# Kernel tuning notes

Hardware: AMD Instinct MI355X
Metric: run time of the kernel (lower is better)

## Reference

```python
import jax, jax.numpy as jnp
import numpy as np

B, T, H, NC = 64, 512, 1000, 2000
WV, PV, IV, TV, MV = 100000, 50, 5, 20, 500
FEAT = 300 + 4 * 50  # 500
EPS = 1e-5


def setup_inputs() -> dict:
    key = jax.random.key(0)
    ks = jax.random.split(key, 32)

    def emb(k, v, d):
        t = jax.random.normal(k, (v, d), jnp.float32) * 0.1
        return t.at[0].set(0.0)  # padding_idx=0

    def unif(k, shape, s):
        return jax.random.uniform(k, shape, jnp.float32, -s, s)

    s = 1.0 / np.sqrt(H)
    inp = {}
    inp['word_idxs'] = jax.random.randint(ks[0], (B, T), 0, WV)
    inp['pos_idxs'] = jax.random.randint(ks[1], (B, T), 0, PV)
    inp['iob_idxs'] = jax.random.randint(ks[2], (B, T), 0, IV)
    inp['type_idxs'] = jax.random.randint(ks[3], (B, T), 0, TV)
    inp['mention_idxs'] = jax.random.randint(ks[4], (B, T), 0, MV)
    lengths = jnp.sort(jax.random.randint(ks[5], (B,), 1, T + 1))[::-1]
    inp['lengths'] = lengths.at[0].set(T)  # descending, max == T
    inp['hidden'] = jnp.zeros((2, B, H), jnp.float32)
    inp['word_emb'] = emb(ks[6], WV, 300)
    inp['pos_emb'] = emb(ks[7], PV, 50)
    inp['iob_emb'] = emb(ks[8], IV, 50)
    inp['type_emb'] = emb(ks[9], TV, 50)
    inp['mention_emb'] = emb(ks[10], MV, 50)
    inp['w_ih_fwd'] = unif(ks[11], (3 * H, FEAT), s)
    inp['w_hh_fwd'] = unif(ks[12], (3 * H, H), s)
    inp['b_ih_fwd'] = unif(ks[13], (3 * H,), s)
    inp['b_hh_fwd'] = unif(ks[14], (3 * H,), s)
    inp['w_ih_bwd'] = unif(ks[15], (3 * H, FEAT), s)
    inp['w_hh_bwd'] = unif(ks[16], (3 * H, H), s)
    inp['b_ih_bwd'] = unif(ks[17], (3 * H,), s)
    inp['b_hh_bwd'] = unif(ks[18], (3 * H,), s)
    inp['lin_w'] = unif(ks[19], (NC, 2 * H), 1.0 / np.sqrt(2 * H))
    inp['lin_b'] = unif(ks[20], (NC,), 1.0 / np.sqrt(2 * H))
    inp['bn_gamma'] = 1.0 + 0.1 * jax.random.normal(ks[21], (NC,), jnp.float32)
    inp['bn_beta'] = 0.1 * jax.random.normal(ks[22], (NC,), jnp.float32)
    inp['bn_mean'] = 0.1 * jax.random.normal(ks[23], (NC,), jnp.float32)
    inp['bn_var'] = jax.random.uniform(ks[24], (NC,), jnp.float32, 0.5, 1.5)
    return inp


def _gru_dir(x_proj, mask, h0, w_hh, b_hh):
    """x_proj: [T,B,3H] precomputed input projections; mask: [T,B] validity."""
    def step(h, tm):
        xp, m = tm
        hp = h @ w_hh.T + b_hh  # [B,3H]
        xr, xz, xn = jnp.split(xp, 3, axis=-1)
        hr, hz, hn = jnp.split(hp, 3, axis=-1)
        r = jax.nn.sigmoid(xr + hr)
        z = jax.nn.sigmoid(xz + hz)
        n = jnp.tanh(xn + r * hn)
        h_new = (1.0 - z) * n + z * h
        h = jnp.where(m[:, None], h_new, h)  # freeze past sequence end (packed semantics)
        return h, None
    hT, _ = jax.lax.scan(step, h0, (x_proj, mask))
    return hT


def reference(word_idxs, pos_idxs, iob_idxs, type_idxs, mention_idxs, lengths, hidden,
              word_emb, pos_emb, iob_emb, type_emb, mention_emb,
              w_ih_fwd, w_hh_fwd, b_ih_fwd, b_hh_fwd,
              w_ih_bwd, w_hh_bwd, b_ih_bwd, b_hh_bwd,
              lin_w, lin_b, bn_gamma, bn_beta, bn_mean, bn_var):
    # multi-embedding concat -> [B,T,500]; eval mode: dropouts identity
    feat = jnp.concatenate([
        word_emb[word_idxs], pos_emb[pos_idxs], iob_emb[iob_idxs],
        type_emb[type_idxs], mention_emb[mention_idxs]], axis=-1)
    valid = (jnp.arange(T)[None, :] < lengths[:, None])  # [B,T]

    # forward direction
    xpf = jnp.einsum('btf,gf->tbg', feat, w_ih_fwd) + b_ih_fwd  # [T,B,3H]
    h_f = _gru_dir(xpf, valid.T, hidden[0], w_hh_fwd, b_hh_fwd)

    # backward direction: reverse the valid portion of each sequence
    rev_idx = jnp.clip(lengths[:, None] - 1 - jnp.arange(T)[None, :], 0, T - 1)  # [B,T]
    feat_r = jnp.take_along_axis(feat, rev_idx[:, :, None], axis=1)
    xpb = jnp.einsum('btf,gf->tbg', feat_r, w_ih_bwd) + b_ih_bwd
    h_b = _gru_dir(xpb, valid.T, hidden[1], w_hh_bwd, b_hh_bwd)

    h_cat = jnp.concatenate([h_f, h_b], axis=-1)  # [B,2H]
    logits = h_cat @ lin_w.T + lin_b
    out = bn_gamma * (logits - bn_mean) * jax.lax.rsqrt(bn_var + EPS) + bn_beta
    hidden_out = jnp.stack([h_f, h_b])  # [2,B,H] like PyTorch GRU final hidden
    return out, hidden_out
```

## Files before the change

### kernel.cpp

```cpp
#include <hip/hip_runtime.h>
#include <hip/hip_bf16.h>

typedef __attribute__((ext_vector_type(8))) short bf16x8;
typedef __attribute__((ext_vector_type(4))) float f32x4;

#define MFMA16(a,b,c) __builtin_amdgcn_mfma_f32_16x16x32_bf16((a),(b),(c),0,0,0)

__device__ __forceinline__ float sigmf(float x){ return 1.f/(1.f + __expf(-x)); }
__device__ __forceinline__ float tanh_fast(float x){
    float e = __expf(-2.f*fabsf(x));
    float t = (1.f-e)/(1.f+e);
    return x < 0.f ? -t : t;
}

#define AS1 __attribute__((address_space(1)))
#define AS3 __attribute__((address_space(3)))
__device__ __forceinline__ void gll16(const void* g, void* l) {
    __builtin_amdgcn_global_load_lds((const AS1 unsigned int*)g, (AS3 unsigned int*)l, 16, 0, 0);
}

__device__ __forceinline__ bf16x8 load16_asm(const __hip_bfloat16* p) {
    bf16x8 v;
    asm volatile("global_load_dwordx4 %0, %1, off" : "=v"(v) : "v"(p));
    return v;
}
__device__ __forceinline__ bf16x8 load16_sc(const __hip_bfloat16* p) {
    bf16x8 v;
    asm volatile("global_load_dwordx4 %0, %1, off sc0 sc1" : "=v"(v) : "v"(p) : "memory");
    return v;
}
__device__ __forceinline__ void store2_sc(__hip_bfloat16* p, float v) {
    __hip_bfloat16 b = __float2bfloat16(v);
    unsigned int u = *reinterpret_cast<unsigned short*>(&b);
    asm volatile("global_store_short %0, %1, off sc0 sc1" :: "v"(p), "v"(u) : "memory");
}
__device__ __forceinline__ void store4_sc(unsigned* p, unsigned v) {
    asm volatile("global_store_dword %0, %1, off sc0 sc1" :: "v"(p), "v"(v) : "memory");
}
__device__ __forceinline__ unsigned poll_sc(const unsigned* p) {
    unsigned v;
    asm volatile("global_load_dword %0, %1, off sc0 sc1\n\ts_waitcnt vmcnt(0)"
                 : "=v"(v) : "v"(p) : "memory");
    return v;
}
__device__ __forceinline__ unsigned ld2_g(const __hip_bfloat16* p) {
    unsigned v;
    asm volatile("global_load_ushort %0, %1, off" : "=v"(v) : "v"(p));
    return v;
}

#define B_   64
#define T_   512
#define H_   1000
#define HP   1024
#define G3   3072
#define NC_  2000
#define FEAT_C 500
#define FEAT_P 512
#define NROWS 32768

#define OFF_FEAT  ((size_t)0)
#define OFF_WIHF  (OFF_FEAT + 33554432ull)
#define OFF_WIHB  (OFF_WIHF + 3145728ull)
#define OFF_WHH   (OFF_WIHB + 3145728ull)
#define OFF_LINW  (OFF_WHH + 12582912ull)
#define OFF_BIHF  (OFF_LINW + 8192000ull)
#define OFF_BIHB  (OFF_BIHF + 12288ull)
#define OFF_BHH   (OFF_BIHB + 12288ull)
#define OFF_XP    (OFF_BHH + 24576ull)
#define OFF_HBF   (OFF_XP + 402653184ull)
#define OFF_HCAT  (OFF_HBF + 524288ull)
#define OFF_BAR   (OFF_HCAT + 262144ull)
#define WS_NEED   (OFF_BAR + 8192ull)

__global__ void cvt_pad_3h(const float* __restrict__ src, __hip_bfloat16* __restrict__ dst,
                           int C, int Cp) {
    size_t i = (size_t)blockIdx.x*blockDim.x + threadIdx.x;
    size_t total = (size_t)G3 * Cp;
    if (i >= total) return;
    int r = (int)(i / Cp), c = (int)(i % Cp);
    int chunk = r >> 10, j = r & 1023;
    float v = (j < H_ && c < C) ? src[((size_t)chunk*H_ + j)*C + c] : 0.f;
    dst[i] = __float2bfloat16(v);
}

__global__ void cvt_pad(const float* __restrict__ src, __hip_bfloat16* __restrict__ dst,
                        int R, int C, int Cp) {
    size_t i = (size_t)blockIdx.x*blockDim.x + threadIdx.x;
    size_t total = (size_t)R * Cp;
    if (i >= total) return;
    int r = (int)(i / Cp), c = (int)(i % Cp);
    float v = (c < C) ? src[(size_t)r*C + c] : 0.f;
    dst[i] = __float2bfloat16(v);
}

__global__ void pad_b3h(const float* __restrict__ src, float* __restrict__ dst) {
    int i = blockIdx.x*blockDim.x + threadIdx.x;
    if (i >= G3) return;
    int chunk = i >> 10, j = i & 1023;
    dst[i] = (j < H_) ? src[chunk*H_ + j] : 0.f;
}

__global__ __launch_bounds__(256)
void embed_k(const int* __restrict__ wi, const int* __restrict__ pi, const int* __restrict__ ii,
             const int* __restrict__ ti, const int* __restrict__ mi,
             const float* __restrict__ we, const float* __restrict__ pe, const float* __restrict__ ie,
             const float* __restrict__ te, const float* __restrict__ me,
             __hip_bfloat16* __restrict__ feat) {
    int r = blockIdx.x;
    int iw = wi[r], ip = pi[r], ib = ii[r], it = ti[r], im = mi[r];
    #pragma unroll
    for (int q = 0; q < 2; ++q) {
        int c = threadIdx.x + q*256;
        float v;
        if      (c < 300) v = we[(size_t)iw*300 + c];
        else if (c < 350) v = pe[ip*50 + (c-300)];
        else if (c < 400) v = ie[ib*50 + (c-350)];
        else if (c < 450) v = te[it*50 + (c-400)];
        else if (c < 500) v = me[im*50 + (c-450)];
        else              v = 0.f;
        feat[(size_t)r*FEAT_P + c] = __float2bfloat16(v);
    }
}

__global__ __launch_bounds__(256)
void gemm_xp(const __hip_bfloat16* __restrict__ feat,
             const __hip_bfloat16* __restrict__ W,
             const float* __restrict__ bias,
             const int* __restrict__ lengths,
             __hip_bfloat16* __restrict__ xp,
             int dir) {
    __shared__ char smem_raw[32768];
    __hip_bfloat16* As = (__hip_bfloat16*)smem_raw;
    __hip_bfloat16* Bs = (__hip_bfloat16*)(smem_raw + 16384);
    const int tid = threadIdx.x;
    const int wave = tid >> 6, lane = tid & 63;
    const int bm = blockIdx.x, bn = blockIdx.y;
    const int wm = wave >> 1, wn = wave & 1;

    int arow_src[4];
    #pragma unroll
    for (int q = 0; q < 4; ++q) {
        int flat = q*256 + tid;
        int row = flat >> 3;
        int r_g = bm*128 + row;
        int t = r_g >> 6, b = r_g & 63;
        int src_t;
        if (dir == 0) src_t = t;
        else { int L = lengths[b]; src_t = L - 1 - t; src_t = src_t < 0 ? 0 : src_t; }
        arow_src[q] = b*T_ + src_t;
    }

    f32x4 acc[4][4];
    #pragma unroll
    for (int i = 0; i < 4; ++i)
        #pragma unroll
        for (int j = 0; j < 4; ++j) acc[i][j] = (f32x4){0.f,0.f,0.f,0.f};

    for (int kt = 0; kt < 8; ++kt) {
        int k0 = kt*64;
        #pragma unroll
        for (int q = 0; q < 4; ++q) {
            int flat = q*256 + tid;
            int row = flat >> 3, c8 = flat & 7;
            gll16(feat + (size_t)arow_src[q]*FEAT_P + k0 + c8*8,
                  As + (q*256 + wave*64)*8);
            gll16(W + (size_t)(bn*128 + row)*FEAT_P + k0 + c8*8,
                  Bs + (q*256 + wave*64)*8);
        }
        __syncthreads();
        #pragma unroll
        for (int ks = 0; ks < 2; ++ks) {
            bf16x8 af[4], bfr[4];
            #pragma unroll
            for (int i = 0; i < 4; ++i)
                af[i] = *(const bf16x8*)(As + (wm*64 + i*16 + (lane&15))*64 + ks*32 + (lane>>4)*8);
            #pragma unroll
            for (int j = 0; j < 4; ++j)
                bfr[j] = *(const bf16x8*)(Bs + (wn*64 + j*16 + (lane&15))*64 + ks*32 + (lane>>4)*8);
            #pragma unroll
            for (int i = 0; i < 4; ++i)
                #pragma unroll
                for (int j = 0; j < 4; ++j)
                    acc[i][j] = MFMA16(af[i], bfr[j], acc[i][j]);
        }
        __syncthreads();
    }

    __hip_bfloat16* Cs = (__hip_bfloat16*)smem_raw;
    #pragma unroll
    for (int j = 0; j < 4; ++j) {
        int col_l = wn*64 + j*16 + (lane & 15);
        float bs = bias[bn*128 + col_l];
        #pragma unroll
        for (int i = 0; i < 4; ++i) {
            #pragma unroll
            for (int r = 0; r < 4; ++r) {
                int row_l = wm*64 + i*16 + (lane>>4)*4 + r;
                Cs[row_l*128 + col_l] = __float2bfloat16(acc[i][j][r] + bs);
            }
        }
    }
    __syncthreads();
    #pragma unroll
    for (int q = 0; q < 8; ++q) {
        int flat = q*256 + tid;
        int row = flat >> 4, c8 = flat & 15;
        bf16x8 v = *(const bf16x8*)(Cs + row*128 + c8*8);
        *(bf16x8*)(xp + (size_t)(bm*128 + row)*G3 + bn*128 + c8*8) = v;
    }
}

__global__ void init_h(const float* __restrict__ hidden, __hip_bfloat16* __restrict__ hbf) {
    int i = blockIdx.x*blockDim.x + threadIdx.x;
    if (i >= 2*B_*HP) return;
    int row = i >> 10, j = i & 1023;
    int dir = row >> 6, b = row & 63;
    float v = (j < H_) ? hidden[((size_t)dir*B_ + b)*H_ + j] : 0.f;
    __hip_bfloat16 bv = __float2bfloat16(v);
    hbf[i] = bv;
    hbf[2*B_*HP + i] = bv;
}

__global__ void bar_init(unsigned* bar) {
    int i = blockIdx.x*blockDim.x + threadIdx.x;
    if (i < 2048) bar[i] = 0u;
}

__global__ __launch_bounds__(512, 2)
void gru_persist(const __hip_bfloat16* __restrict__ whh,
                 const float* __restrict__ bhh,
                 const __hip_bfloat16* __restrict__ xp,
                 const int* __restrict__ lengths,
                 const float* __restrict__ hidden,
                 __hip_bfloat16* __restrict__ hbf,
                 __hip_bfloat16* __restrict__ hcat,
                 float* __restrict__ hid_o,
                 unsigned* __restrict__ bar) {
    __shared__ float part[2][4][3][256];
    const int blk = blockIdx.x;
    const int r8  = blk & 7, q8 = blk >> 3;
    const int g   = r8 >> 1;
    const int dir = g >> 1, bh = g & 1;
    const int ug  = q8*2 + (r8 & 1);
    const int w    = threadIdx.x >> 6;
    const int lane = threadIdx.x & 63;
    const int bg  = w >> 2;
    const int kh  = w & 3;
    const int u   = lane & 15;
    const int rg  = lane >> 4;

    const int j   = ug*16 + u;
    const int bA  = bh*32 + bg*16 + u;
    const int bF  = bh*32 + bg*16 + rg*4 + kh;
    const int myLen  = lengths[bF];
    const int lenBlk = lengths[bh*32];

    unsigned* cntg  = bar + g*512;
    unsigned* flagp = bar + g*512 + 256;

    const float bhr = bhh[dir*G3 + j];
    const float bhz = bhh[dir*G3 + HP + j];
    const float bhn = bhh[dir*G3 + 2*HP + j];
    float hreg = (j < H_) ? hidden[((size_t)dir*B_ + bF)*H_ + j] : 0.f;

    bf16x8 wf0[8], wf1[8], wf2[8];
    {
        const __hip_bfloat16* wb = whh + (size_t)dir*G3*HP + (size_t)j*HP + kh*256 + rg*8;
        #pragma unroll
        for (int ks = 0; ks < 8; ++ks) {
            wf0[ks] = load16_asm(wb + ks*32);
            wf1[ks] = load16_asm(wb + (size_t)HP*HP + ks*32);
            wf2[ks] = load16_asm(wb + (size_t)2*HP*HP + ks*32);
        }
        asm volatile("s_waitcnt vmcnt(0)" ::: "memory");
        __builtin_amdgcn_sched_barrier(0);
    }

    const size_t hrowA = (size_t)(dir*B_ + bA)*HP + kh*256 + rg*8;
    const size_t hidxF = (size_t)(dir*B_ + bF)*HP + j;
    const size_t xbase = (size_t)dir*NROWS*G3 + (size_t)bF*G3 + j;

    unsigned pxr, pxz, pxn;
    {
        const __hip_bfloat16* x0 = xp + xbase;
        pxr = ld2_g(x0); pxz = ld2_g(x0 + HP); pxn = ld2_g(x0 + 2*HP);
    }

    for (int t = 0; t < lenBlk; ++t) {
        const int cur = t & 1, prev = cur ^ 1;
        const __hip_bfloat16* ha = hbf + (size_t)prev*2*B_*HP + hrowA;
        bf16x8 af[8];
        #pragma unroll
        for (int ks = 0; ks < 8; ++ks) af[ks] = load16_sc(ha + ks*32);
        asm volatile("s_waitcnt vmcnt(0)" ::: "memory");
        __builtin_amdgcn_sched_barrier(0);

        f32x4 a0 = {0.f,0.f,0.f,0.f}, a1 = {0.f,0.f,0.f,0.f}, a2 = {0.f,0.f,0.f,0.f};
        #pragma unroll
        for (int ks = 0; ks < 8; ++ks) {
            a0 = MFMA16(af[ks], wf0[ks], a0);
            a1 = MFMA16(af[ks], wf1[ks], a1);
            a2 = MFMA16(af[ks], wf2[ks], a2);
        }

        float xr = __uint_as_float(pxr << 16);
        float xz = __uint_as_float(pxz << 16);
        float xn = __uint_as_float(pxn << 16);

        *(f32x4*)&part[bg][kh][0][lane*4] = a0;
        *(f32x4*)&part[bg][kh][1][lane*4] = a1;
        *(f32x4*)&part[bg][kh][2][lane*4] = a2;
        __syncthreads();
        float sr = 0.f, sz = 0.f, sn = 0.f;
        #pragma unroll
        for (int q = 0; q < 4; ++q) {
            sr += part[bg][q][0][lane*4 + kh];
            sz += part[bg][q][1][lane*4 + kh];
            sn += part[bg][q][2][lane*4 + kh];
        }
        float rr = sigmf(xr + sr + bhr);
        float zz = sigmf(xz + sz + bhz);
        float nn = tanh_fast(xn + rr*(sn + bhn));
        float hnew = (t < myLen) ? ((1.f - zz)*nn + zz*hreg) : hreg;
        hreg = hnew;
        store2_sc(hbf + (size_t)cur*2*B_*HP + hidxF, hnew);
        asm volatile("s_waitcnt vmcnt(0)" ::: "memory");
        __syncthreads();

        if (t + 1 < lenBlk) {
            {
                const __hip_bfloat16* xnp = xp + xbase + (size_t)(t+1)*B_*G3;
                pxr = ld2_g(xnp); pxz = ld2_g(xnp + HP); pxn = ld2_g(xnp + 2*HP);
            }
            if (w == 0) {
                const unsigned tgt = (unsigned)(t + 1);
                if (lane == 0) atomicAdd(cntg + (ug >> 3)*32, 1u);
                if (ug == 0) {
                    for (;;) {
                        unsigned v = poll_sc(cntg + (lane & 7)*32);
                        if (__all((int)(v >= 8u*tgt))) break;
                    }
                    if (lane == 0) store4_sc(flagp, tgt);
                } else {
                    if (lane == 0) { while (poll_sc(flagp) < tgt) { } }
                }
            }
            __syncthreads();
        }
    }

    if (j < H_) {
        hid_o[((size_t)dir*B_ + bF)*H_ + j] = hreg;
        hcat[(size_t)bF*2048 + dir*H_ + j] = __float2bfloat16(hreg);
    } else {
        hcat[(size_t)bF*2048 + 2000 + dir*24 + (j - H_)] = __float2bfloat16(0.f);
    }
}

__global__ __launch_bounds__(256)
void lin_bn_k(const __hip_bfloat16* __restrict__ hcat,
              const __hip_bfloat16* __restrict__ linw,
              const float* __restrict__ lin_b, const float* __restrict__ gamma,
              const float* __restrict__ beta, const float* __restrict__ mean,
              const float* __restrict__ var,
              float* __restrict__ out) {
    __shared__ __hip_bfloat16 wlds[16*2056];
    const int n0 = blockIdx.x*16;
    const int tid = threadIdx.x;
    #pragma unroll
    for (int q = 0; q < 16; ++q) {
        int flat8 = q*256 + tid;
        int row = flat8 >> 8, c8 = flat8 & 255;
        bf16x8 v = *(const bf16x8*)(linw + (size_t)(n0+row)*2048 + c8*8);
        *(bf16x8*)(wlds + row*2056 + c8*8) = v;
    }
    __syncthreads();
    const int wave = tid >> 6, lane = tid & 63;
    const int mrow = wave*16 + (lane & 15);
    f32x4 acc = {0.f,0.f,0.f,0.f};
    for (int ks = 0; ks < 64; ++ks) {
        bf16x8 a = *(const bf16x8*)(hcat + (size_t)mrow*2048 + ks*32 + (lane>>4)*8);
        bf16x8 b = *(const bf16x8*)(wlds + (lane&15)*2056 + ks*32 + (lane>>4)*8);
        acc = MFMA16(a, b, acc);
    }
    const int c = n0 + (lane & 15);
    const float g = gamma[c], bt = beta[c], mn = mean[c], lb = lin_b[c];
    const float iv = rsqrtf(var[c] + 1e-5f);
    #pragma unroll
    for (int r = 0; r < 4; ++r) {
        int b_ = wave*16 + (lane>>4)*4 + r;
        float logit = acc[r] + lb;
        out[(size_t)b_*NC_ + c] = g*(logit - mn)*iv + bt;
    }
}

extern "C" void kernel_launch(void* const* d_in, const int* in_sizes, int n_in,
                              void* d_out, int out_size, void* d_ws, size_t ws_size,
                              hipStream_t stream) {
    const int*   wi      = (const int*)d_in[0];
    const int*   pi      = (const int*)d_in[1];
    const int*   ii      = (const int*)d_in[2];
    const int*   ti      = (const int*)d_in[3];
    const int*   mi      = (const int*)d_in[4];
    const int*   lengths = (const int*)d_in[5];
    const float* hidden  = (const float*)d_in[6];
    const float* we      = (const float*)d_in[7];
    const float* pe      = (const float*)d_in[8];
    const float* ie      = (const float*)d_in[9];
    const float* te      = (const float*)d_in[10];
    const float* me      = (const float*)d_in[11];
    const float* w_ih_f  = (const float*)d_in[12];
    const float* w_hh_f  = (const float*)d_in[13];
    const float* b_ih_f  = (const float*)d_in[14];
    const float* b_hh_f  = (const float*)d_in[15];
    const float* w_ih_b  = (const float*)d_in[16];
    const float* w_hh_b  = (const float*)d_in[17];
    const float* b_ih_b  = (const float*)d_in[18];
    const float* b_hh_b  = (const float*)d_in[19];
    const float* lin_w   = (const float*)d_in[20];
    const float* lin_b   = (const float*)d_in[21];
    const float* gamma   = (const float*)d_in[22];
    const float* beta    = (const float*)d_in[23];
    const float* mean    = (const float*)d_in[24];
    const float* var     = (const float*)d_in[25];
    float* out = (float*)d_out;

    if (ws_size < WS_NEED) return;

    char* ws = (char*)d_ws;
    __hip_bfloat16* FEAT = (__hip_bfloat16*)(ws + OFF_FEAT);
    __hip_bfloat16* WIHF = (__hip_bfloat16*)(ws + OFF_WIHF);
    __hip_bfloat16* WIHB = (__hip_bfloat16*)(ws + OFF_WIHB);
    __hip_bfloat16* WHH  = (__hip_bfloat16*)(ws + OFF_WHH);
    __hip_bfloat16* LINW = (__hip_bfloat16*)(ws + OFF_LINW);
    float* BIHF = (float*)(ws + OFF_BIHF);
    float* BIHB = (float*)(ws + OFF_BIHB);
    float* BHH  = (float*)(ws + OFF_BHH);
    __hip_bfloat16* XP   = (__hip_bfloat16*)(ws + OFF_XP);
    __hip_bfloat16* HBF  = (__hip_bfloat16*)(ws + OFF_HBF);
    __hip_bfloat16* HCAT = (__hip_bfloat16*)(ws + OFF_HCAT);
    unsigned* BAR = (unsigned*)(ws + OFF_BAR);
    float* HIDO = out + (size_t)B_*NC_;

    cvt_pad_3h<<<(G3*512 + 255)/256, 256, 0, stream>>>(w_ih_f, WIHF, FEAT_C, FEAT_P);
    cvt_pad_3h<<<(G3*512 + 255)/256, 256, 0, stream>>>(w_ih_b, WIHB, FEAT_C, FEAT_P);
    cvt_pad_3h<<<(G3*1024 + 255)/256, 256, 0, stream>>>(w_hh_f, WHH, H_, HP);
    cvt_pad_3h<<<(G3*1024 + 255)/256, 256, 0, stream>>>(w_hh_b, WHH + (size_t)G3*HP, H_, HP);
    cvt_pad<<<(NC_*2048 + 255)/256, 256, 0, stream>>>(lin_w, LINW, NC_, NC_, 2048);
    pad_b3h<<<(G3 + 255)/256, 256, 0, stream>>>(b_ih_f, BIHF);
    pad_b3h<<<(G3 + 255)/256, 256, 0, stream>>>(b_ih_b, BIHB);
    pad_b3h<<<(G3 + 255)/256, 256, 0, stream>>>(b_hh_f, BHH);
    pad_b3h<<<(G3 + 255)/256, 256, 0, stream>>>(b_hh_b, BHH + G3);

    embed_k<<<NROWS, 256, 0, stream>>>(wi, pi, ii, ti, mi, we, pe, ie, te, me, FEAT);

    dim3 gg(NROWS/128, G3/128);
    gemm_xp<<<gg, 256, 0, stream>>>(FEAT, WIHF, BIHF, lengths, XP, 0);
    gemm_xp<<<gg, 256, 0, stream>>>(FEAT, WIHB, BIHB, lengths, XP + (size_t)NROWS*G3, 1);

    init_h<<<(2*B_*HP + 255)/256, 256, 0, stream>>>(hidden, HBF);
    bar_init<<<8, 256, 0, stream>>>(BAR);
    {
        void* args[] = { (void*)&WHH, (void*)&BHH, (void*)&XP, (void*)&lengths,
                         (void*)&hidden, (void*)&HBF, (void*)&HCAT, (void*)&HIDO, (void*)&BAR };
        hipLaunchCooperativeKernel((const void*)gru_persist, dim3(256), dim3(512),
                                   args, 0, stream);
    }

    lin_bn_k<<<NC_/16, 256, 0, stream>>>(HCAT, LINW, lin_b, gamma, beta, mean, var, out);
}
```

Before: 2.847 ms.

## Replace grid barrier with per-element step-tagged hidden state polling

Each hidden element is now stored as a 32-bit word that packs the bf16 value in the high half and the timestep tag in the low half. Consumers poll the tagged words until every tag matches the expected step, which removes the atomic counter and flag barrier between steps. Consumers therefore wait only on the data they read instead of a full group barrier. The cost is twice the bytes per hidden-state read, repeated polling of those reads, and extra unpacking ALU. The hidden buffer also reuses the feature workspace region, which is assumed dead by the time the GRU runs.

After: 5.688 ms. 99.8% more time.

```diff
diff --git a/kernel.cpp b/kernel.cpp
--- a/kernel.cpp
+++ b/kernel.cpp
@@ -3,6 +3,7 @@
 
 typedef __attribute__((ext_vector_type(8))) short bf16x8;
 typedef __attribute__((ext_vector_type(4))) float f32x4;
+typedef __attribute__((ext_vector_type(4))) unsigned u32x4;
 
 #define MFMA16(a,b,c) __builtin_amdgcn_mfma_f32_16x16x32_bf16((a),(b),(c),0,0,0)
 
@@ -24,24 +25,13 @@
     asm volatile("global_load_dwordx4 %0, %1, off" : "=v"(v) : "v"(p));
     return v;
 }
-__device__ __forceinline__ bf16x8 load16_sc(const __hip_bfloat16* p) {
-    bf16x8 v;
+__device__ __forceinline__ u32x4 load16u_sc(const unsigned* p) {
+    u32x4 v;
     asm volatile("global_load_dwordx4 %0, %1, off sc0 sc1" : "=v"(v) : "v"(p) : "memory");
     return v;
 }
-__device__ __forceinline__ void store2_sc(__hip_bfloat16* p, float v) {
-    __hip_bfloat16 b = __float2bfloat16(v);
-    unsigned int u = *reinterpret_cast<unsigned short*>(&b);
-    asm volatile("global_store_short %0, %1, off sc0 sc1" :: "v"(p), "v"(u) : "memory");
-}
 __device__ __forceinline__ void store4_sc(unsigned* p, unsigned v) {
     asm volatile("global_store_dword %0, %1, off sc0 sc1" :: "v"(p), "v"(v) : "memory");
-}
-__device__ __forceinline__ unsigned poll_sc(const unsigned* p) {
-    unsigned v;
-    asm volatile("global_load_dword %0, %1, off sc0 sc1\n\ts_waitcnt vmcnt(0)"
-                 : "=v"(v) : "v"(p) : "memory");
-    return v;
 }
 __device__ __forceinline__ unsigned ld2_g(const __hip_bfloat16* p) {
     unsigned v;
@@ -60,6 +50,7 @@
 #define NROWS 32768
 
 #define OFF_FEAT  ((size_t)0)
+#define OFF_HX    OFF_FEAT
 #define OFF_WIHF  (OFF_FEAT + 33554432ull)
 #define OFF_WIHB  (OFF_WIHF + 3145728ull)
 #define OFF_WHH   (OFF_WIHB + 3145728ull)
@@ -68,10 +59,8 @@
 #define OFF_BIHB  (OFF_BIHF + 12288ull)
 #define OFF_BHH   (OFF_BIHB + 12288ull)
 #define OFF_XP    (OFF_BHH + 24576ull)
-#define OFF_HBF   (OFF_XP + 402653184ull)
-#define OFF_HCAT  (OFF_HBF + 524288ull)
-#define OFF_BAR   (OFF_HCAT + 262144ull)
-#define WS_NEED   (OFF_BAR + 8192ull)
+#define OFF_HCAT  (OFF_XP + 402653184ull)
+#define WS_NEED   (OFF_HCAT + 262144ull)
 
 __global__ void cvt_pad_3h(const float* __restrict__ src, __hip_bfloat16* __restrict__ dst,
                            int C, int Cp) {
@@ -211,20 +200,16 @@
     }
 }
 
-__global__ void init_h(const float* __restrict__ hidden, __hip_bfloat16* __restrict__ hbf) {
+__global__ void init_h(const float* __restrict__ hidden, unsigned* __restrict__ hx) {
     int i = blockIdx.x*blockDim.x + threadIdx.x;
     if (i >= 2*B_*HP) return;
     int row = i >> 10, j = i & 1023;
     int dir = row >> 6, b = row & 63;
     float v = (j < H_) ? hidden[((size_t)dir*B_ + b)*H_ + j] : 0.f;
     __hip_bfloat16 bv = __float2bfloat16(v);
-    hbf[i] = bv;
-    hbf[2*B_*HP + i] = bv;
-}
-
-__global__ void bar_init(unsigned* bar) {
-    int i = blockIdx.x*blockDim.x + threadIdx.x;
-    if (i < 2048) bar[i] = 0u;
+    unsigned word = ((unsigned)*reinterpret_cast<unsigned short*>(&bv)) << 16;
+    hx[i] = word;
+    hx[2*B_*HP + i] = word;
 }
 
 __global__ __launch_bounds__(512, 2)
@@ -233,10 +218,9 @@
                  const __hip_bfloat16* __restrict__ xp,
                  const int* __restrict__ lengths,
                  const float* __restrict__ hidden,
-                 __hip_bfloat16* __restrict__ hbf,
+                 unsigned* __restrict__ hx,
                  __hip_bfloat16* __restrict__ hcat,
-                 float* __restrict__ hid_o,
-                 unsigned* __restrict__ bar) {
+                 float* __restrict__ hid_o) {
     __shared__ float part[2][4][3][256];
     const int blk = blockIdx.x;
     const int r8  = blk & 7, q8 = blk >> 3;
@@ -256,9 +240,6 @@
     const int myLen  = lengths[bF];
     const int lenBlk = lengths[bh*32];
 
-    unsigned* cntg  = bar + g*512;
-    unsigned* flagp = bar + g*512 + 256;
-
     const float bhr = bhh[dir*G3 + j];
     const float bhz = bhh[dir*G3 + HP + j];
     const float bhn = bhh[dir*G3 + 2*HP + j];
@@ -288,13 +269,35 @@
     }
 
     for (int t = 0; t < lenBlk; ++t) {
-        const int cur = t & 1, prev = cur ^ 1;
-        const __hip_bfloat16* ha = hbf + (size_t)prev*2*B_*HP + hrowA;
+        const unsigned* hrd = hx + (size_t)((t+1)&1)*2*B_*HP + hrowA;
+        const unsigned tgt = (unsigned)t;
+        u32x4 wv[16];
+        for (;;) {
+            #pragma unroll
+            for (int ks = 0; ks < 8; ++ks) {
+                wv[2*ks]   = load16u_sc(hrd + ks*32);
+                wv[2*ks+1] = load16u_sc(hrd + ks*32 + 4);
+            }
+            asm volatile("s_waitcnt vmcnt(0)" ::: "memory");
+            unsigned acc = 0;
+            #pragma unroll
+            for (int q = 0; q < 16; ++q)
+                #pragma unroll
+                for (int e = 0; e < 4; ++e) acc |= (wv[q][e] ^ tgt) & 0xFFFFu;
+            if (__all((int)(acc == 0))) break;
+        }
+        __builtin_amdgcn_sched_barrier(0);
+
         bf16x8 af[8];
         #pragma unroll
-        for (int ks = 0; ks < 8; ++ks) af[ks] = load16_sc(ha + ks*32);
-        asm volatile("s_waitcnt vmcnt(0)" ::: "memory");
-        __builtin_amdgcn_sched_barrier(0);
+        for (int ks = 0; ks < 8; ++ks) {
+            union { unsigned u4[4]; bf16x8 v; } cv;
+            cv.u4[0] = (wv[2*ks][0]   >> 16) | (wv[2*ks][1]   & 0xFFFF0000u);
+            cv.u4[1] = (wv[2*ks][2]   >> 16) | (wv[2*ks][3]   & 0xFFFF0000u);
+            cv.u4[2] = (wv[2*ks+1][0] >> 16) | (wv[2*ks+1][1] & 0xFFFF0000u);
+            cv.u4[3] = (wv[2*ks+1][2] >> 16) | (wv[2*ks+1][3] & 0xFFFF0000u);
+            af[ks] = cv.v;
+        }
 
         f32x4 a0 = {0.f,0.f,0.f,0.f}, a1 = {0.f,0.f,0.f,0.f}, a2 = {0.f,0.f,0.f,0.f};
         #pragma unroll
@@ -319,35 +322,24 @@
             sz += part[bg][q][1][lane*4 + kh];
             sn += part[bg][q][2][lane*4 + kh];
         }
+
         float rr = sigmf(xr + sr + bhr);
         float zz = sigmf(xz + sz + bhz);
         float nn = tanh_fast(xn + rr*(sn + bhn));
         float hnew = (t < myLen) ? ((1.f - zz)*nn + zz*hreg) : hreg;
         hreg = hnew;
-        store2_sc(hbf + (size_t)cur*2*B_*HP + hidxF, hnew);
-        asm volatile("s_waitcnt vmcnt(0)" ::: "memory");
+        {
+            __hip_bfloat16 hb = __float2bfloat16(hnew);
+            unsigned word = (((unsigned)*reinterpret_cast<unsigned short*>(&hb)) << 16)
+                            | (unsigned)(t + 1);
+            store4_sc(hx + (size_t)(t & 1)*2*B_*HP + hidxF, word);
+        }
+
+        if (t + 1 < lenBlk) {
+            const __hip_bfloat16* xnp = xp + xbase + (size_t)(t+1)*B_*G3;
+            pxr = ld2_g(xnp); pxz = ld2_g(xnp + HP); pxn = ld2_g(xnp + 2*HP);
+        }
         __syncthreads();
-
-        if (t + 1 < lenBlk) {
-            {
-                const __hip_bfloat16* xnp = xp + xbase + (size_t)(t+1)*B_*G3;
-                pxr = ld2_g(xnp); pxz = ld2_g(xnp + HP); pxn = ld2_g(xnp + 2*HP);
-            }
-            if (w == 0) {
-                const unsigned tgt = (unsigned)(t + 1);
-                if (lane == 0) atomicAdd(cntg + (ug >> 3)*32, 1u);
-                if (ug == 0) {
-                    for (;;) {
-                        unsigned v = poll_sc(cntg + (lane & 7)*32);
-                        if (__all((int)(v >= 8u*tgt))) break;
-                    }
-                    if (lane == 0) store4_sc(flagp, tgt);
-                } else {
-                    if (lane == 0) { while (poll_sc(flagp) < tgt) { } }
-                }
-            }
-            __syncthreads();
-        }
     }
 
     if (j < H_) {
@@ -430,6 +422,7 @@
 
     char* ws = (char*)d_ws;
     __hip_bfloat16* FEAT = (__hip_bfloat16*)(ws + OFF_FEAT);
+    unsigned*       HX   = (unsigned*)(ws + OFF_HX);
     __hip_bfloat16* WIHF = (__hip_bfloat16*)(ws + OFF_WIHF);
     __hip_bfloat16* WIHB = (__hip_bfloat16*)(ws + OFF_WIHB);
     __hip_bfloat16* WHH  = (__hip_bfloat16*)(ws + OFF_WHH);
@@ -438,9 +431,7 @@
     float* BIHB = (float*)(ws + OFF_BIHB);
     float* BHH  = (float*)(ws + OFF_BHH);
     __hip_bfloat16* XP   = (__hip_bfloat16*)(ws + OFF_XP);
-    __hip_bfloat16* HBF  = (__hip_bfloat16*)(ws + OFF_HBF);
     __hip_bfloat16* HCAT = (__hip_bfloat16*)(ws + OFF_HCAT);
-    unsigned* BAR = (unsigned*)(ws + OFF_BAR);
     float* HIDO = out + (size_t)B_*NC_;
 
     cvt_pad_3h<<<(G3*512 + 255)/256, 256, 0, stream>>>(w_ih_f, WIHF, FEAT_C, FEAT_P);
@@ -459,11 +450,10 @@
     gemm_xp<<<gg, 256, 0, stream>>>(FEAT, WIHF, BIHF, lengths, XP, 0);
     gemm_xp<<<gg, 256, 0, stream>>>(FEAT, WIHB, BIHB, lengths, XP + (size_t)NROWS*G3, 1);
 
-    init_h<<<(2*B_*HP + 255)/256, 256, 0, stream>>>(hidden, HBF);
-    bar_init<<<8, 256, 0, stream>>>(BAR);
+    init_h<<<(2*B_*HP + 255)/256, 256, 0, stream>>>(hidden, HX);
     {
         void* args[] = { (void*)&WHH, (void*)&BHH, (void*)&XP, (void*)&lengths,
-                         (void*)&hidden, (void*)&HBF, (void*)&HCAT, (void*)&HIDO, (void*)&BAR };
+                         (void*)&hidden, (void*)&HX, (void*)&HCAT, (void*)&HIDO };
         hipLaunchCooperativeKernel((const void*)gru_persist, dim3(256), dim3(512),
                                    args, 0, stream);
     }
```
